# Kernel tuning notes

Hardware: AMD Instinct MI355X
Metric: run time of the kernel (lower is better)

## Reference

```python
import jax, jax.numpy as jnp
import numpy as np
import math

D_MODEL = 512; NHEAD = 8; D_FF = 2048
DS_HEADS = 4; DS_DEPTH = 156; EPS = 1e-5
B = 128; N = 300; M = 300


def _ln(x, g, b):
    m = x.mean(-1, keepdims=True)
    v = ((x - m) ** 2).mean(-1, keepdims=True)
    return (x - m) / jnp.sqrt(v + EPS) * g + b


def _mish(x):
    return x * jnp.tanh(jax.nn.softplus(x))


def _mha(xq, xk, xv, in_w, in_b, out_w, out_b, nhead):
    D = xq.shape[-1]; dh = D // nhead
    wq, wk, wv = jnp.split(in_w, 3, axis=0)
    bq, bk, bv = jnp.split(in_b, 3)
    def proj(x, w, b):
        y = x @ w.T + b
        Bm, Nn, _ = y.shape
        return y.reshape(Bm, Nn, nhead, dh).transpose(0, 2, 1, 3)
    q, k, v = proj(xq, wq, bq), proj(xk, wk, bk), proj(xv, wv, bv)
    s = jnp.einsum('bhqd,bhkd->bhqk', q, k) / math.sqrt(dh)
    p = jax.nn.softmax(s, axis=-1)
    o = jnp.einsum('bhqk,bhkd->bhqd', p, v)
    Bm, _, Nn, _ = o.shape
    o = o.transpose(0, 2, 1, 3).reshape(Bm, Nn, D)
    return o @ out_w.T + out_b


def _custom_weight(p):
    # sequential kinematic-tree averaging on the post-softmax [...,24,24] matrix
    def upd(p, i, j, si, sj):
        return p.at[..., i, j].set((p[..., i, j] + p[..., si, sj]) * 0.5)
    p = upd(p, 0, 6, 0, 3); p = upd(p, 6, 0, 3, 0)
    p = upd(p, 0, 9, 0, 6); p = upd(p, 9, 0, 6, 0)
    for idx in (12, 13, 14):
        p = upd(p, 0, idx, 0, 9); p = upd(p, idx, 0, 9, 0)
    for s, tgt in ((13, 16), (14, 17), (12, 15)):
        p = upd(p, 0, tgt, 0, s); p = upd(p, tgt, 0, s, 0)
    return p


def _ds_attn(x, qk_w, v_w, lw, lb):
    Bm, Nn, _ = x.shape
    comb = jnp.einsum('bnf,fx->bnx', x, qk_w)
    q, k = jnp.split(comb, 2, axis=2)
    v = jnp.einsum('bnf,fx->bnx', x, v_w)
    def heads(y):
        return y.reshape(Bm, Nn, DS_HEADS, DS_DEPTH).transpose(0, 2, 1, 3)
    q, k, v = heads(q), heads(k), heads(v)  # [B,H,N,156]
    qs = q[..., 3:147].reshape(Bm, DS_HEADS, Nn, 24, 6)
    ks = k[..., 3:147].reshape(Bm, DS_HEADS, Nn, 24, 6)
    vs = v[..., 3:147].reshape(Bm, DS_HEADS, Nn, 24, 6)
    s = jnp.einsum('bhnij,bhnkj->bhnik', qs, ks) / math.sqrt(6.0)
    p = _custom_weight(jax.nn.softmax(s, axis=-1))
    o = jnp.einsum('bhnik,bhnkj->bhnij', p, vs).reshape(Bm, DS_HEADS, Nn, 144)
    v = v.at[..., 3:147].set(o)
    v = v.transpose(0, 2, 1, 3).reshape(Bm, Nn, DS_HEADS * DS_DEPTH)
    return v @ lw.T + lb


def _align(x_d, t, w, b):
    tt = t + x_d.mean(axis=-2)           # [B,D]
    h = _mish(tt) @ w.T + b              # [B,2D]
    weight, bias = jnp.split(h, 2, axis=-1)
    return (weight[:, None, :] + 1.0) * x_d + bias[:, None, :]


def _forward(tgt, memory, t, qk_w, v_w, ds_lw, ds_lb,
             ta_in_w, ta_in_b, ta_out_w, ta_out_b,
             ca_in_w, ca_in_b, ca_out_w, ca_out_b,
             l1_w, l1_b, l2_w, l2_b,
             n1_g, n1_b, n2_g, n2_b, n3_g, n3_b, n4_g, n4_b,
             a1_w, a1_b, a2_w, a2_b, a3_w, a3_b):
    x = tgt
    x = x + _ds_attn(_ln(x, n1_g, n1_b), qk_w, v_w, ds_lw, ds_lb)
    xn = _ln(x, n2_g, n2_b)
    x2 = _mha(xn, xn, xn, ta_in_w, ta_in_b, ta_out_w, ta_out_b, NHEAD)
    x = x + _align(x2, t, a1_w, a1_b)
    x3 = _mha(_ln(x, n3_g, n3_b), memory, memory, ca_in_w, ca_in_b, ca_out_w, ca_out_b, NHEAD)
    x = x + _align(x3, t, a2_w, a2_b)
    xn4 = _ln(x, n4_g, n4_b)
    x4 = jax.nn.relu(xn4 @ l1_w.T + l1_b) @ l2_w.T + l2_b
    x = x + _align(x4, t, a3_w, a3_b)
    return x


def setup_inputs():
    key = jax.random.key(0)
    ks = iter(jax.random.split(key, 64))
    def nrm(shape, s=0.02):
        return jax.random.normal(next(ks), shape, dtype=jnp.float32) * s
    z = lambda *shape: jnp.zeros(shape, jnp.float32)
    o = lambda *shape: jnp.ones(shape, jnp.float32)
    D = D_MODEL
    inp = {
        'tgt': jax.random.normal(next(ks), (B, N, D), dtype=jnp.float32),
        'memory': jax.random.normal(next(ks), (B, M, D), dtype=jnp.float32),
        't': jax.random.normal(next(ks), (B, D), dtype=jnp.float32),
        'qk_w': nrm((D, 2 * DS_DEPTH * DS_HEADS)),
        'v_w': nrm((D, DS_DEPTH * DS_HEADS)),
        'ds_lw': nrm((D, DS_DEPTH * DS_HEADS)), 'ds_lb': z(D),
        'ta_in_w': nrm((3 * D, D)), 'ta_in_b': z(3 * D),
        'ta_out_w': nrm((D, D)), 'ta_out_b': z(D),
        'ca_in_w': nrm((3 * D, D)), 'ca_in_b': z(3 * D),
        'ca_out_w': nrm((D, D)), 'ca_out_b': z(D),
        'l1_w': nrm((D_FF, D)), 'l1_b': z(D_FF),
        'l2_w': nrm((D, D_FF)), 'l2_b': z(D),
        'n1_g': o(D), 'n1_b': z(D), 'n2_g': o(D), 'n2_b': z(D),
        'n3_g': o(D), 'n3_b': z(D), 'n4_g': o(D), 'n4_b': z(D),
        'a1_w': nrm((2 * D, D)), 'a1_b': z(2 * D),
        'a2_w': nrm((2 * D, D)), 'a2_b': z(2 * D),
        'a3_w': nrm((2 * D, D)), 'a3_b': z(2 * D),
        'cond_drop_prob': 0,
    }
    return inp


def reference(tgt, memory, t, qk_w, v_w, ds_lw, ds_lb,
              ta_in_w, ta_in_b, ta_out_w, ta_out_b,
              ca_in_w, ca_in_b, ca_out_w, ca_out_b,
              l1_w, l1_b, l2_w, l2_b,
              n1_g, n1_b, n2_g, n2_b, n3_g, n3_b, n4_g, n4_b,
              a1_w, a1_b, a2_w, a2_b, a3_w, a3_b, cond_drop_prob):
    # cond_drop_prob is unused in the torch forward body (dropout eval mode)
    return _forward(tgt, memory, t, qk_w, v_w, ds_lw, ds_lb,
                    ta_in_w, ta_in_b, ta_out_w, ta_out_b,
                    ca_in_w, ca_in_b, ca_out_w, ca_out_b,
                    l1_w, l1_b, l2_w, l2_b,
                    n1_g, n1_b, n2_g, n2_b, n3_g, n3_b, n4_g, n4_b,
                    a1_w, a1_b, a2_w, a2_b, a3_w, a3_b)
```

## Files before the change

kernel.cpp:

```cpp
#include <hip/hip_runtime.h>
#include <math.h>

#define DEV __device__ __forceinline__

static constexpr int BB   = 128;
static constexpr int NN   = 300;
static constexpr int DM   = 512;

typedef __attribute__((ext_vector_type(8))) short short8;
typedef __attribute__((ext_vector_type(4))) float f32x4;

DEV unsigned short f2bf(float f) {
  unsigned u = __float_as_uint(f);
  unsigned r = (u + 0x7fffu + ((u >> 16) & 1u)) >> 16;
  return (unsigned short)r;
}
DEV float bf2f(unsigned short s) { return __uint_as_float((unsigned)s << 16); }
DEV unsigned pack_trunc(float a, float b) {
  return (__float_as_uint(a) >> 16) | (__float_as_uint(b) & 0xffff0000u);
}

DEV void gld16(const void* g, void* l) {
  __builtin_amdgcn_global_load_lds(
      (const __attribute__((address_space(1))) unsigned int*)g,
      (__attribute__((address_space(3))) unsigned int*)l,
      16, 0, 0);
}

__global__ __launch_bounds__(256) void ln_kernel(
    const float* __restrict__ X, const float* __restrict__ g,
    const float* __restrict__ b, unsigned short* __restrict__ Y, int rows)
{
  int wv = threadIdx.x >> 6, lane = threadIdx.x & 63;
  int row = blockIdx.x * 4 + wv;
  if (row >= rows) return;
  const float* xp = X + (size_t)row * DM;
  float v[8]; float s = 0.f, s2 = 0.f;
#pragma unroll
  for (int j = 0; j < 8; j++) {
    v[j] = xp[lane + 64 * j]; s += v[j]; s2 += v[j] * v[j];
  }
#pragma unroll
  for (int o = 32; o >= 1; o >>= 1) { s += __shfl_xor(s, o); s2 += __shfl_xor(s2, o); }
  float mean = s * (1.f / 512.f);
  float var  = s2 * (1.f / 512.f) - mean * mean;
  float rstd = rsqrtf(var + 1e-5f);
  unsigned short* yp = Y + (size_t)row * DM;
#pragma unroll
  for (int j = 0; j < 8; j++) {
    int c = lane + 64 * j;
    yp[c] = f2bf((v[j] - mean) * rstd * g[c] + b[c]);
  }
}

__global__ __launch_bounds__(256) void align_ln(
    float* __restrict__ X, const float* __restrict__ Y,
    const float* __restrict__ H,
    const float* __restrict__ g, const float* __restrict__ bb,
    unsigned short* __restrict__ XN)
{
  int wv = threadIdx.x >> 6, lane = threadIdx.x & 63;
  int row = blockIdx.x * 4 + wv;
  int b = row / NN;
  float* xp = X + (size_t)row * DM;
  const float* yp = Y + (size_t)row * DM;
  const float* hw = H + (size_t)b * 1024;
  const float* hb = hw + 512;
  float v[8]; float s = 0.f, s2 = 0.f;
#pragma unroll
  for (int j = 0; j < 8; j++) {
    int c = lane + 64 * j;
    float xv = xp[c] + (hw[c] + 1.f) * yp[c] + hb[c];
    v[j] = xv; s += xv; s2 += xv * xv;
  }
#pragma unroll
  for (int j = 0; j < 8; j++) xp[lane + 64 * j] = v[j];
#pragma unroll
  for (int o = 32; o >= 1; o >>= 1) { s += __shfl_xor(s, o); s2 += __shfl_xor(s2, o); }
  float mean = s * (1.f / 512.f);
  float var  = s2 * (1.f / 512.f) - mean * mean;
  float rstd = rsqrtf(var + 1e-5f);
  unsigned short* yn = XN + (size_t)row * DM;
#pragma unroll
  for (int j = 0; j < 8; j++) {
    int c = lane + 64 * j;
    yn[c] = f2bf((v[j] - mean) * rstd * g[c] + bb[c]);
  }
}

__global__ __launch_bounds__(256) void cvt_bf16(
    const float* __restrict__ in, unsigned short* __restrict__ out, int n4)
{
  int i = blockIdx.x * 256 + threadIdx.x;
  if (i >= n4) return;
  float4 v = ((const float4*)in)[i];
  union { unsigned short s[4]; uint2 u; } o;
  o.s[0] = f2bf(v.x); o.s[1] = f2bf(v.y); o.s[2] = f2bf(v.z); o.s[3] = f2bf(v.w);
  *(uint2*)&out[(size_t)i * 4] = o.u;
}

__global__ __launch_bounds__(256) void cvt_pad_bf16(
    const float* __restrict__ in, unsigned short* __restrict__ out,
    int R, int C, int Cpad)
{
  int idx = blockIdx.x * 256 + threadIdx.x;
  int r = idx / Cpad, c = idx % Cpad;
  if (r >= R) return;
  out[idx] = (c < C) ? f2bf(in[(size_t)r * C + c]) : (unsigned short)0;
}

__global__ __launch_bounds__(256) void transpose_bf16(
    const float* __restrict__ in, unsigned short* __restrict__ out,
    int R, int Ccols, int Cpad)
{
  __shared__ float t[32][33];
  int c0 = blockIdx.x * 32, r0 = blockIdx.y * 32;
  int x = threadIdx.x & 31, y = threadIdx.x >> 5;
#pragma unroll
  for (int dy = 0; dy < 32; dy += 8) {
    int r = r0 + y + dy, c = c0 + x;
    t[y + dy][x] = (r < R && c < Ccols) ? in[(size_t)r * Ccols + c] : 0.f;
  }
  __syncthreads();
#pragma unroll
  for (int dy = 0; dy < 32; dy += 8) {
    int c = c0 + y + dy, r = r0 + x;
    if (c < Cpad && r < R) out[(size_t)c * R + r] = f2bf(t[x][y + dy]);
  }
}

template<int EPI>
__global__ __launch_bounds__(256) void gemm_bb(
    const unsigned short* __restrict__ A, int lda,
    const unsigned short* __restrict__ W, int ldw,
    const float* __restrict__ bias,
    const float* __restrict__ R, int ldr,
    void* __restrict__ Cv, int ldc,
    int M, int K, int NC, int coloff)
{
  __shared__ __align__(16) unsigned short As[128 * 32];
  __shared__ __align__(16) unsigned short Bs[128 * 32];
  const int tid = threadIdx.x;
  const int wave = tid >> 6, lane = tid & 63;
  const int wr = wave >> 1, wc = wave & 1;
  const int quad = lane >> 4, l16 = lane & 15;

  const unsigned nx = gridDim.x, nwg = nx * gridDim.y;
  const unsigned orig = blockIdx.y * nx + blockIdx.x;
  const unsigned qq = nwg >> 3, rr = nwg & 7;
  const unsigned xcd = orig & 7, idx = orig >> 3;
  const unsigned swz = (xcd < rr) ? (xcd * (qq + 1) + idx)
                                  : (rr * (qq + 1) + (xcd - rr) * qq + idx);
  const int n0 = (int)(swz % nx) * 128;
  const int m0 = (int)(swz / nx) * 128;

  int ra = m0 + (tid >> 2);
  int ra0 = (ra      >= M) ? M - 1 : ra;
  int ra1 = (ra + 64 >= M) ? M - 1 : ra + 64;
  const unsigned short* a0 = A + (size_t)ra0 * lda + (tid & 3) * 8;
  const unsigned short* a1 = A + (size_t)ra1 * lda + (tid & 3) * 8;
  const unsigned short* b0 = W + (size_t)(n0 + (tid >> 2)) * ldw + (tid & 3) * 8;
  const unsigned short* b1 = b0 + (size_t)64 * ldw;
  unsigned short* dA0 = &As[wave * 512];
  unsigned short* dA1 = &As[2048 + wave * 512];
  unsigned short* dB0 = &Bs[wave * 512];
  unsigned short* dB1 = &Bs[2048 + wave * 512];

  f32x4 acc[4][4];
#pragma unroll
  for (int i = 0; i < 4; i++)
#pragma unroll
    for (int j = 0; j < 4; j++) acc[i][j] = (f32x4){0.f, 0.f, 0.f, 0.f};

  for (int k0 = 0; k0 < K; k0 += 32) {
    gld16(a0 + k0, dA0);
    gld16(a1 + k0, dA1);
    gld16(b0 + k0, dB0);
    gld16(b1 + k0, dB1);
    __syncthreads();
    short8 af[4], bq[4];
#pragma unroll
    for (int i = 0; i < 4; i++)
      af[i] = *(const short8*)&As[(wr * 64 + i * 16 + l16) * 32 + quad * 8];
#pragma unroll
    for (int j = 0; j < 4; j++)
      bq[j] = *(const short8*)&Bs[(wc * 64 + j * 16 + l16) * 32 + quad * 8];
#pragma unroll
    for (int i = 0; i < 4; i++)
#pragma unroll
      for (int j = 0; j < 4; j++)
        acc[i][j] = __builtin_amdgcn_mfma_f32_16x16x32_bf16(af[i], bq[j], acc[i][j], 0, 0, 0);
    __syncthreads();
  }

#pragma unroll
  for (int i = 0; i < 4; i++) {
    int rbase = m0 + wr * 64 + i * 16 + quad * 4;
#pragma unroll
    for (int r = 0; r < 4; r++) {
      int row = rbase + r;
      if (row < M) {
        size_t rowc = (size_t)row * ldc;
#pragma unroll
        for (int j = 0; j < 4; j++) {
          int col = n0 + wc * 64 + j * 16 + l16;
          if (col < NC) {
            float e = acc[i][j][r];
            if (EPI == 1 || EPI == 2 || EPI == 3 || EPI == 7) e += bias[col];
            if (EPI == 3) e += R[(size_t)row * ldr + col];
            if (EPI == 2) {
              ((unsigned short*)Cv)[rowc + col] = f2bf(fmaxf(e, 0.f));
            } else if (EPI == 7) {
              int cc = col + coloff;
              int sec = cc >> 9, hh = (cc >> 6) & 7, dh = cc & 63;
              ((unsigned short*)Cv)[(((size_t)(sec * 8 + hh)) * M + row) * 64 + dh] = f2bf(e);
            } else if (EPI == 8) {
              if (col < 1248)
                ((unsigned short*)Cv)[(size_t)row * 1248 + col] = f2bf(e);
              else if (col >= 1280)
                ((unsigned short*)(void*)R)[(size_t)row * 640 + (col - 1280)] = f2bf(e);
            } else {
              ((float*)Cv)[rowc + col] = e;
            }
          }
        }
      }
    }
  }
}

__global__ __launch_bounds__(256) void ds_attn_kernel(
    const unsigned short* __restrict__ COMB, unsigned short* __restrict__ V)
{
  __shared__ float ks[4][2][24][6];
  __shared__ float vs[4][2][24][6];
  int wv = threadIdx.x >> 6, lane = threadIdx.x & 63;
  int half = lane >> 5, i = lane & 31;
  int u  = blockIdx.x * 4 + wv;
  int bn = u >> 1, hp = u & 1;
  int h  = hp * 2 + half;
  size_t cbase = (size_t)bn * 1248 + h * 156 + 3;
  size_t vbase = (size_t)bn * 640  + h * 156 + 3;

  float q[6];
  if (i < 24) {
#pragma unroll
    for (int j = 0; j < 6; j++) {
      q[j]                 = bf2f(COMB[cbase + i * 6 + j]);
      ks[wv][half][i][j]   = bf2f(COMB[cbase + 624 + i * 6 + j]);
      vs[wv][half][i][j]   = bf2f(V[vbase + i * 6 + j]);
    }
  } else {
#pragma unroll
    for (int j = 0; j < 6; j++) q[j] = 0.f;
  }
  __syncthreads();

  float p[24];
#pragma unroll
  for (int k = 0; k < 24; k++) p[k] = 0.f;

  if (i < 24) {
    float mx = -1e30f;
#pragma unroll
    for (int k = 0; k < 24; k++) {
      float s = 0.f;
#pragma unroll
      for (int j = 0; j < 6; j++) s += q[j] * ks[wv][half][k][j];
      s *= 0.4082482904638631f;
      p[k] = s; mx = fmaxf(mx, s);
    }
    float sum = 0.f;
#pragma unroll
    for (int k = 0; k < 24; k++) { p[k] = __expf(p[k] - mx); sum += p[k]; }
    float inv = 1.f / sum;
#pragma unroll
    for (int k = 0; k < 24; k++) p[k] *= inv;
  }

  {
    float c = p[0];
    float t;
    t = __shfl(c, 3, 32);  if (i == 6) c = (c + t) * 0.5f;
    t = __shfl(c, 6, 32);  if (i == 9) c = (c + t) * 0.5f;
    t = __shfl(c, 9, 32);  if (i >= 12 && i <= 14) c = (c + t) * 0.5f;
    int src = (i >= 3) ? (i - 3) : 0;
    t = __shfl(c, src, 32); if (i >= 15 && i <= 17) c = (c + t) * 0.5f;
    p[0] = c;
  }
  if (i == 0) {
    p[6]  = (p[6]  + p[3])  * 0.5f;
    p[9]  = (p[9]  + p[6])  * 0.5f;
    p[12] = (p[12] + p[9])  * 0.5f;
    p[13] = (p[13] + p[9])  * 0.5f;
    p[14] = (p[14] + p[9])  * 0.5f;
    p[16] = (p[16] + p[13]) * 0.5f;
    p[17] = (p[17] + p[14]) * 0.5f;
    p[15] = (p[15] + p[12]) * 0.5f;
  }

  if (i < 24) {
    float o[6] = {0.f, 0.f, 0.f, 0.f, 0.f, 0.f};
#pragma unroll
    for (int k = 0; k < 24; k++) {
#pragma unroll
      for (int j = 0; j < 6; j++) o[j] += p[k] * vs[wv][half][k][j];
    }
#pragma unroll
    for (int j = 0; j < 6; j++) V[vbase + i * 6 + j] = f2bf(o[j]);
  }
}

__global__ __launch_bounds__(512) void mha_mfma(
    const unsigned short* __restrict__ QKV3, unsigned short* __restrict__ Op,
    int rowsT, float scale)
{
  __shared__ __align__(16) unsigned short Ksh[304 * 72];
  __shared__ __align__(16) unsigned short Vt[64 * 328];
  __shared__ __align__(16) unsigned short Pt[8][16 * 68];
  const int bh = blockIdx.x, b = bh >> 3, h = bh & 7;
  const int tid = threadIdx.x, wv = tid >> 6, lane = tid & 63;
  const int quad = lane >> 4, l16 = lane & 15;
  const unsigned short* Qp = QKV3 + ((size_t)h        * rowsT + b * NN) * 64;
  const unsigned short* Kp = QKV3 + ((size_t)(8 + h)  * rowsT + b * NN) * 64;
  const unsigned short* Vp = QKV3 + ((size_t)(16 + h) * rowsT + b * NN) * 64;

  for (int f = tid; f < 304 * 8; f += 512) {
    int rk = f >> 3, c8 = (f & 7) * 8;
    short8 w;
    if (rk < 300) {
      w = *(const short8*)(Kp + f * 8);
    } else {
      union { uint4 u; short8 s; } z; z.u = make_uint4(0u, 0u, 0u, 0u); w = z.s;
    }
    *(short8*)&Ksh[rk * 72 + c8] = w;
  }
  for (int f = tid; f < 64 * 164; f += 512) {
    int d = f & 63, s0 = (f >> 6) * 2;
    unsigned w = 0u;
    if (s0 < 300) {
      unsigned short v0 = Vp[s0 * 64 + d];
      unsigned short v1 = (s0 + 1 < 300) ? Vp[(s0 + 1) * 64 + d] : (unsigned short)0;
      w = (unsigned)v0 | ((unsigned)v1 << 16);
    }
    *(unsigned*)&Vt[d * 328 + s0] = w;
  }
  __syncthreads();

  unsigned short* pt = &Pt[wv][0];

  for (int qt = wv; qt < 19; qt += 8) {
    int qr = qt * 16 + l16; if (qr > 299) qr = 299;
    short8 qf[2];
    qf[0] = *(const short8*)(Qp + qr * 64 + quad * 8);
    qf[1] = *(const short8*)(Qp + qr * 64 + 32 + quad * 8);

    f32x4 sacc[19];
#pragma unroll
    for (int t = 0; t < 19; t++) {
      short8 k0 = *(const short8*)&Ksh[(t * 16 + l16) * 72 + quad * 8];
      short8 k1 = *(const short8*)&Ksh[(t * 16 + l16) * 72 + 32 + quad * 8];
      f32x4 a = (f32x4){0.f, 0.f, 0.f, 0.f};
      a = __builtin_amdgcn_mfma_f32_16x16x32_bf16(k0, qf[0], a, 0, 0, 0);
      a = __builtin_amdgcn_mfma_f32_16x16x32_bf16(k1, qf[1], a, 0, 0, 0);
      sacc[t] = a;
    }

    float mx = -1e30f;
#pragma unroll
    for (int t = 0; t < 19; t++)
#pragma unroll
      for (int r = 0; r < 4; r++) mx = fmaxf(mx, sacc[t][r]);
    mx = fmaxf(mx, __shfl_xor(mx, 16));
    mx = fmaxf(mx, __shfl_xor(mx, 32));
    float sum = 0.f;
#pragma unroll
    for (int t = 0; t < 19; t++) {
#pragma unroll
      for (int r = 0; r < 4; r++) {
        float p = __expf((sacc[t][r] - mx) * scale);
        if (t == 18 && quad == 3) p = 0.f;
        sacc[t][r] = p; sum += p;
      }
    }
    sum += __shfl_xor(sum, 16);
    sum += __shfl_xor(sum, 32);
    float inv = 1.f / sum;

    f32x4 oacc[4];
#pragma unroll
    for (int dt = 0; dt < 4; dt++) oacc[dt] = (f32x4){0.f, 0.f, 0.f, 0.f};
#pragma unroll
    for (int c = 0; c < 10; c++) {
#pragma unroll
      for (int tic = 0; tic < 2; tic++) {
        int t = 2 * c + tic;
        unsigned w0 = 0u, w1 = 0u;
        if (t < 19) {
          w0 = pack_trunc(sacc[t][0], sacc[t][1]);
          w1 = pack_trunc(sacc[t][2], sacc[t][3]);
        }
        *(unsigned*)&pt[l16 * 68 + tic * 16 + quad * 4]     = w0;
        *(unsigned*)&pt[l16 * 68 + tic * 16 + quad * 4 + 2] = w1;
      }
      short8 pa = *(const short8*)&pt[l16 * 68 + quad * 8];
#pragma unroll
      for (int dt = 0; dt < 4; dt++) {
        short8 vb = *(const short8*)&Vt[(dt * 16 + l16) * 328 + c * 32 + quad * 8];
        oacc[dt] = __builtin_amdgcn_mfma_f32_16x16x32_bf16(pa, vb, oacc[dt], 0, 0, 0);
      }
    }

#pragma unroll
    for (int r = 0; r < 4; r++) {
      float iv = __shfl(inv, quad * 4 + r);
#pragma unroll
      for (int dt = 0; dt < 4; dt++)
        pt[(quad * 4 + r) * 68 + dt * 16 + l16] = f2bf(oacc[dt][r] * iv);
    }
#pragma unroll
    for (int rep = 0; rep < 2; rep++) {
      int idx = rep * 64 + lane;
      int rl = idx >> 3, seg = idx & 7;
      int row = qt * 16 + rl;
      uint4 w = *(const uint4*)&pt[rl * 68 + seg * 8];
      if (row < 300)
        *(uint4*)(Op + (size_t)(b * NN + row) * DM + h * 64 + seg * 8) = w;
    }
  }
}

__global__ __launch_bounds__(256) void colmean_mish(
    const float* __restrict__ Y, const float* __restrict__ tvec,
    unsigned short* __restrict__ mm)
{
  int g = blockIdx.x * 256 + threadIdx.x;
  int b = g >> 9, d = g & 511;
  const float* yp = Y + (size_t)b * NN * DM + d;
  float s = 0.f;
  for (int n = 0; n < NN; n++) s += yp[(size_t)n * DM];
  float v = tvec[g] + s * (1.f / 300.f);
  float sp = (v > 20.f) ? v : log1pf(__expf(v));
  mm[g] = f2bf(v * tanhf(sp));
}

__global__ __launch_bounds__(256) void align_apply(
    float* __restrict__ X, const float* __restrict__ Y,
    const float* __restrict__ H)
{
  int idx = blockIdx.x * 256 + threadIdx.x;
  int row = idx >> 7;
  int d4  = (idx & 127) * 4;
  int b   = row / NN;
  float4 y = *(const float4*)&Y[(size_t)row * DM + d4];
  float4 x = *(const float4*)&X[(size_t)row * DM + d4];
  const float* hw = H + (size_t)b * 1024 + d4;
  const float* hb = hw + 512;
  x.x += (hw[0] + 1.f) * y.x + hb[0];
  x.y += (hw[1] + 1.f) * y.y + hb[1];
  x.z += (hw[2] + 1.f) * y.z + hb[2];
  x.w += (hw[3] + 1.f) * y.w + hb[3];
  *(float4*)&X[(size_t)row * DM + d4] = x;
}

extern "C" void kernel_launch(void* const* d_in, const int* in_sizes, int n_in,
                              void* d_out, int out_size, void* d_ws, size_t ws_size,
                              hipStream_t stream)
{
  const float* tgt      = (const float*)d_in[0];
  const float* memory   = (const float*)d_in[1];
  const float* tvec     = (const float*)d_in[2];
  const float* qk_w     = (const float*)d_in[3];
  const float* v_w      = (const float*)d_in[4];
  const float* ds_lw    = (const float*)d_in[5];
  const float* ds_lb    = (const float*)d_in[6];
  const float* ta_in_w  = (const float*)d_in[7];
  const float* ta_in_b  = (const float*)d_in[8];
  const float* ta_out_w = (const float*)d_in[9];
  const float* ta_out_b = (const float*)d_in[10];
  const float* ca_in_w  = (const float*)d_in[11];
  const float* ca_in_b  = (const float*)d_in[12];
  const float* ca_out_w = (const float*)d_in[13];
  const float* ca_out_b = (const float*)d_in[14];
  const float* l1_w     = (const float*)d_in[15];
  const float* l1_b     = (const float*)d_in[16];
  const float* l2_w     = (const float*)d_in[17];
  const float* l2_b     = (const float*)d_in[18];
  const float* n1_g = (const float*)d_in[19]; const float* n1_b = (const float*)d_in[20];
  const float* n2_g = (const float*)d_in[21]; const float* n2_b = (const float*)d_in[22];
  const float* n3_g = (const float*)d_in[23]; const float* n3_b = (const float*)d_in[24];
  const float* n4_g = (const float*)d_in[25]; const float* n4_b = (const float*)d_in[26];
  const float* a1_w = (const float*)d_in[27]; const float* a1_b = (const float*)d_in[28];
  const float* a2_w = (const float*)d_in[29]; const float* a2_b = (const float*)d_in[30];
  const float* a3_w = (const float*)d_in[31]; const float* a3_b = (const float*)d_in[32];

  const size_t W_W2  = 1920ULL * 512 * 2;
  const size_t W_TAI = 1536ULL * 512 * 2;
  const size_t W_TAO = 512ULL  * 512 * 2;
  const size_t W_CAI = 1536ULL * 512 * 2;
  const size_t W_CAO = 512ULL  * 512 * 2;
  const size_t W_L1  = 2048ULL * 512 * 2;
  const size_t W_L2  = 512ULL  * 2048 * 2;
  const size_t W_DSL = 512ULL  * 640 * 2;
  const size_t W_AX  = 1024ULL * 512 * 2;
  const size_t W_MEM = (size_t)BB * NN * 512 * 2;
  const size_t fixedB = W_W2 + W_TAI + W_TAO + W_CAI + W_CAO
                      + W_L1 + W_L2 + W_DSL + 3 * W_AX + W_MEM;
  const size_t per_b = 300ULL * (1024 + 4096 + 1280 + 2048) + 1024 + 4096;
  int Bc = 128;
  while (Bc > 16 && fixedB + (size_t)Bc * per_b > ws_size) Bc >>= 1;
  const int rows = Bc * NN;
  const int mB   = (rows + 127) / 128;
  const int aB   = (Bc + 127) / 128;
  const int nchunks = BB / Bc;

  char* p = (char*)d_ws;
  unsigned short* W2h   = (unsigned short*)p; p += W_W2;
  unsigned short* taiWh = (unsigned short*)p; p += W_TAI;
  unsigned short* taoWh = (unsigned short*)p; p += W_TAO;
  unsigned short* caiWh = (unsigned short*)p; p += W_CAI;
  unsigned short* caoWh = (unsigned short*)p; p += W_CAO;
  unsigned short* l1Wh  = (unsigned short*)p; p += W_L1;
  unsigned short* l2Wh  = (unsigned short*)p; p += W_L2;
  unsigned short* dslWh = (unsigned short*)p; p += W_DSL;
  unsigned short* a1Wh  = (unsigned short*)p; p += W_AX;
  unsigned short* a2Wh  = (unsigned short*)p; p += W_AX;
  unsigned short* a3Wh  = (unsigned short*)p; p += W_AX;
  unsigned short* memh  = (unsigned short*)p; p += W_MEM;
  unsigned short* XNh   = (unsigned short*)p; p += (size_t)rows * 512 * 2;
  char* SCRB = p;                             p += (size_t)rows * 4096;
  unsigned short* Vdsh  = (unsigned short*)p; p += (size_t)rows * 640 * 2;
  float* Yb  = (float*)p; p += (size_t)rows * 512 * 4;
  unsigned short* MMh = (unsigned short*)p;   p += (size_t)Bc * 512 * 2;
  float* Hb  = (float*)p;

  unsigned short* COMBh = (unsigned short*)SCRB;
  unsigned short* QKV3  = (unsigned short*)SCRB;
  unsigned short* T2h   = (unsigned short*)SCRB;

  dim3 thr(256);

  transpose_bf16<<<dim3(40, 16), thr, 0, stream>>>(qk_w, W2h, 512, 1248, 1280);
  transpose_bf16<<<dim3(20, 16), thr, 0, stream>>>(v_w,  W2h + 1280 * 512, 512, 624, 640);
  cvt_pad_bf16<<<dim3(512 * 640 / 256), thr, 0, stream>>>(ds_lw, dslWh, 512, 624, 640);
  auto cvt = [&](const float* src, unsigned short* dst, size_t n) {
    int n4 = (int)(n / 4);
    cvt_bf16<<<dim3((n4 + 255) / 256), thr, 0, stream>>>(src, dst, n4);
  };
  cvt(ta_in_w,  taiWh, 1536ULL * 512);
  cvt(ta_out_w, taoWh, 512ULL * 512);
  cvt(ca_in_w,  caiWh, 1536ULL * 512);
  cvt(ca_out_w, caoWh, 512ULL * 512);
  cvt(l1_w,     l1Wh,  2048ULL * 512);
  cvt(l2_w,     l2Wh,  512ULL * 2048);
  cvt(a1_w,     a1Wh,  1024ULL * 512);
  cvt(a2_w,     a2Wh,  1024ULL * 512);
  cvt(a3_w,     a3Wh,  1024ULL * 512);
  cvt(memory,   memh,  (size_t)BB * NN * 512);

  for (int c = 0; c < nchunks; ++c) {
    const size_t roff = (size_t)c * Bc * NN * DM;
    const float* tgtC = tgt    + roff;
    const float* tC   = tvec   + (size_t)c * Bc * 512;
    const unsigned short* memhC = memh + roff;
    float*       XC   = (float*)d_out + roff;

    ln_kernel<<<rows / 4, thr, 0, stream>>>(tgtC, n1_g, n1_b, XNh, rows);
    gemm_bb<8><<<dim3(15, mB), thr, 0, stream>>>(XNh, 512, W2h, 512, nullptr, (const float*)Vdsh, 0, COMBh, 1248, rows, 512, 1920, 0);
    ds_attn_kernel<<<rows / 2, thr, 0, stream>>>(COMBh, Vdsh);
    gemm_bb<3><<<dim3(4, mB),  thr, 0, stream>>>(Vdsh, 640, dslWh, 640, ds_lb, tgtC, 512, XC, 512, rows, 640, 512, 0);

    ln_kernel<<<rows / 4, thr, 0, stream>>>(XC, n2_g, n2_b, XNh, rows);
    gemm_bb<7><<<dim3(12, mB), thr, 0, stream>>>(XNh, 512, taiWh, 512, ta_in_b, nullptr, 0, QKV3, 0, rows, 512, 1536, 0);
    mha_mfma<<<Bc * 8, 512, 0, stream>>>(QKV3, XNh, rows, 0.125f);
    gemm_bb<1><<<dim3(4, mB),  thr, 0, stream>>>(XNh, 512, taoWh, 512, ta_out_b, nullptr, 0, Yb, 512, rows, 512, 512, 0);
    colmean_mish<<<Bc * 2, thr, 0, stream>>>(Yb, tC, MMh);
    gemm_bb<1><<<dim3(8, aB),  thr, 0, stream>>>(MMh, 512, a1Wh, 512, a1_b, nullptr, 0, Hb, 1024, Bc, 512, 1024, 0);
    align_ln<<<rows / 4, thr, 0, stream>>>(XC, Yb, Hb, n3_g, n3_b, XNh);

    gemm_bb<7><<<dim3(4, mB),  thr, 0, stream>>>(XNh, 512, caiWh, 512, ca_in_b, nullptr, 0, QKV3, 0, rows, 512, 512, 0);
    gemm_bb<7><<<dim3(8, mB),  thr, 0, stream>>>(memhC, 512, caiWh + 512 * 512, 512, ca_in_b + 512, nullptr, 0, QKV3, 0, rows, 512, 1024, 512);
    mha_mfma<<<Bc * 8, 512, 0, stream>>>(QKV3, XNh, rows, 0.125f);
    gemm_bb<1><<<dim3(4, mB),  thr, 0, stream>>>(XNh, 512, caoWh, 512, ca_out_b, nullptr, 0, Yb, 512, rows, 512, 512, 0);
    colmean_mish<<<Bc * 2, thr, 0, stream>>>(Yb, tC, MMh);
    gemm_bb<1><<<dim3(8, aB),  thr, 0, stream>>>(MMh, 512, a2Wh, 512, a2_b, nullptr, 0, Hb, 1024, Bc, 512, 1024, 0);
    align_ln<<<rows / 4, thr, 0, stream>>>(XC, Yb, Hb, n4_g, n4_b, XNh);

    gemm_bb<2><<<dim3(16, mB), thr, 0, stream>>>(XNh, 512, l1Wh, 512, l1_b, nullptr, 0, T2h, 2048, rows, 512, 2048, 0);
    gemm_bb<1><<<dim3(4, mB),  thr, 0, stream>>>(T2h, 2048, l2Wh, 2048, l2_b, nullptr, 0, Yb, 512, rows, 2048, 512, 0);
    colmean_mish<<<Bc * 2, thr, 0, stream>>>(Yb, tC, MMh);
    gemm_bb<1><<<dim3(8, aB),  thr, 0, stream>>>(MMh, 512, a3Wh, 512, a3_b, nullptr, 0, Hb, 1024, Bc, 512, 1024, 0);
    align_apply<<<rows / 2, thr, 0, stream>>>(XC, Yb, Hb);
  }
}
```

Baseline: 2.340 ms.

## Double-buffer GEMM LDS tiles and stage Q in LDS for attention

The bf16 GEMM now uses two LDS buffers so the async global-to-LDS load of the next K-slice is issued before computing the current one, hiding load latency behind MFMA work. The MHA kernel also copies Q into shared memory alongside K and wraps its MFMA loops in s_setprio to favour matrix issue. The costs are twice the GEMM LDS footprint, which may reduce occupancy, and about 44KB more LDS in the attention kernel. The GEMM loop steps K by 64, which assumes K is a multiple of 64.

```diff
diff --git a/kernel.cpp b/kernel.cpp
--- a/kernel.cpp
+++ b/kernel.cpp
@@ -138,8 +138,8 @@
     void* __restrict__ Cv, int ldc,
     int M, int K, int NC, int coloff)
 {
-  __shared__ __align__(16) unsigned short As[128 * 32];
-  __shared__ __align__(16) unsigned short Bs[128 * 32];
+  __shared__ __align__(16) unsigned short As[2][128 * 32];
+  __shared__ __align__(16) unsigned short Bs[2][128 * 32];
   const int tid = threadIdx.x;
   const int wave = tid >> 6, lane = tid & 63;
   const int wr = wave >> 1, wc = wave & 1;
@@ -161,10 +161,6 @@
   const unsigned short* a1 = A + (size_t)ra1 * lda + (tid & 3) * 8;
   const unsigned short* b0 = W + (size_t)(n0 + (tid >> 2)) * ldw + (tid & 3) * 8;
   const unsigned short* b1 = b0 + (size_t)64 * ldw;
-  unsigned short* dA0 = &As[wave * 512];
-  unsigned short* dA1 = &As[2048 + wave * 512];
-  unsigned short* dB0 = &Bs[wave * 512];
-  unsigned short* dB1 = &Bs[2048 + wave * 512];
 
   f32x4 acc[4][4];
 #pragma unroll
@@ -172,24 +168,35 @@
 #pragma unroll
     for (int j = 0; j < 4; j++) acc[i][j] = (f32x4){0.f, 0.f, 0.f, 0.f};
 
-  for (int k0 = 0; k0 < K; k0 += 32) {
-    gld16(a0 + k0, dA0);
-    gld16(a1 + k0, dA1);
-    gld16(b0 + k0, dB0);
-    gld16(b1 + k0, dB1);
-    __syncthreads();
+  auto STAGE = [&](int buf, int k0) {
+    gld16(a0 + k0, &As[buf][wave * 512]);
+    gld16(a1 + k0, &As[buf][2048 + wave * 512]);
+    gld16(b0 + k0, &Bs[buf][wave * 512]);
+    gld16(b1 + k0, &Bs[buf][2048 + wave * 512]);
+  };
+  auto COMPUTE = [&](int buf) {
     short8 af[4], bq[4];
 #pragma unroll
     for (int i = 0; i < 4; i++)
-      af[i] = *(const short8*)&As[(wr * 64 + i * 16 + l16) * 32 + quad * 8];
+      af[i] = *(const short8*)&As[buf][(wr * 64 + i * 16 + l16) * 32 + quad * 8];
 #pragma unroll
     for (int j = 0; j < 4; j++)
-      bq[j] = *(const short8*)&Bs[(wc * 64 + j * 16 + l16) * 32 + quad * 8];
+      bq[j] = *(const short8*)&Bs[buf][(wc * 64 + j * 16 + l16) * 32 + quad * 8];
 #pragma unroll
     for (int i = 0; i < 4; i++)
 #pragma unroll
       for (int j = 0; j < 4; j++)
         acc[i][j] = __builtin_amdgcn_mfma_f32_16x16x32_bf16(af[i], bq[j], acc[i][j], 0, 0, 0);
+  };
+
+  STAGE(0, 0);
+  __syncthreads();
+  for (int k0 = 0; k0 < K; k0 += 64) {
+    STAGE(1, k0 + 32);
+    COMPUTE(0);
+    __syncthreads();
+    if (k0 + 64 < K) STAGE(0, k0 + 64);
+    COMPUTE(1);
     __syncthreads();
   }
 
@@ -316,6 +323,7 @@
     int rowsT, float scale)
 {
   __shared__ __align__(16) unsigned short Ksh[304 * 72];
+  __shared__ __align__(16) unsigned short Qsh[304 * 72];
   __shared__ __align__(16) unsigned short Vt[64 * 328];
   __shared__ __align__(16) unsigned short Pt[8][16 * 68];
   const int bh = blockIdx.x, b = bh >> 3, h = bh & 7;
@@ -327,13 +335,16 @@
 
   for (int f = tid; f < 304 * 8; f += 512) {
     int rk = f >> 3, c8 = (f & 7) * 8;
-    short8 w;
+    short8 wk, wq;
     if (rk < 300) {
-      w = *(const short8*)(Kp + f * 8);
+      wk = *(const short8*)(Kp + f * 8);
+      wq = *(const short8*)(Qp + f * 8);
     } else {
-      union { uint4 u; short8 s; } z; z.u = make_uint4(0u, 0u, 0u, 0u); w = z.s;
-    }
-    *(short8*)&Ksh[rk * 72 + c8] = w;
+      union { uint4 u; short8 s; } z; z.u = make_uint4(0u, 0u, 0u, 0u);
+      wk = z.s; wq = z.s;
+    }
+    *(short8*)&Ksh[rk * 72 + c8] = wk;
+    *(short8*)&Qsh[rk * 72 + c8] = wq;
   }
   for (int f = tid; f < 64 * 164; f += 512) {
     int d = f & 63, s0 = (f >> 6) * 2;
@@ -350,12 +361,13 @@
   unsigned short* pt = &Pt[wv][0];
 
   for (int qt = wv; qt < 19; qt += 8) {
-    int qr = qt * 16 + l16; if (qr > 299) qr = 299;
+    int qr = qt * 16 + l16;
     short8 qf[2];
-    qf[0] = *(const short8*)(Qp + qr * 64 + quad * 8);
-    qf[1] = *(const short8*)(Qp + qr * 64 + 32 + quad * 8);
+    qf[0] = *(const short8*)&Qsh[qr * 72 + quad * 8];
+    qf[1] = *(const short8*)&Qsh[qr * 72 + 32 + quad * 8];
 
     f32x4 sacc[19];
+    __builtin_amdgcn_s_setprio(1);
 #pragma unroll
     for (int t = 0; t < 19; t++) {
       short8 k0 = *(const short8*)&Ksh[(t * 16 + l16) * 72 + quad * 8];
@@ -365,6 +377,7 @@
       a = __builtin_amdgcn_mfma_f32_16x16x32_bf16(k1, qf[1], a, 0, 0, 0);
       sacc[t] = a;
     }
+    __builtin_amdgcn_s_setprio(0);
 
     float mx = -1e30f;
 #pragma unroll
@@ -404,11 +417,13 @@
         *(unsigned*)&pt[l16 * 68 + tic * 16 + quad * 4 + 2] = w1;
       }
       short8 pa = *(const short8*)&pt[l16 * 68 + quad * 8];
+      __builtin_amdgcn_s_setprio(1);
 #pragma unroll
       for (int dt = 0; dt < 4; dt++) {
         short8 vb = *(const short8*)&Vt[(dt * 16 + l16) * 328 + c * 32 + quad * 8];
         oacc[dt] = __builtin_amdgcn_mfma_f32_16x16x32_bf16(pa, vb, oacc[dt], 0, 0, 0);
       }
+      __builtin_amdgcn_s_setprio(0);
     }
 
 #pragma unroll
```

Result: faster. 1.926 ms (-17.7%).
